# Kernel tuning notes

Hardware: AMD Instinct MI355X
Metric: run time of the kernel (lower is better)

## Reference

```python
import jax, jax.numpy as jnp
import numpy as np

N, C, K, B, G = 32768, 128, 16, 4, 8
SCALE, BASE = 2.0, 10000.0

def _bn(x, gamma, beta, eps=1e-5):
    # torch BatchNorm1d (training): stats over all axes except channel (last)
    axes = tuple(range(x.ndim - 1))
    mean = x.mean(axes)
    var = x.var(axes)
    return (x - mean) / jnp.sqrt(var + eps) * gamma + beta

def _cayley_rope(x, coord, S_param):
    c = x.shape[-1]
    S = jnp.triu(S_param, 1)
    S = S - S.T
    I = jnp.eye(c, dtype=x.dtype)
    P = jnp.linalg.solve(I + S, I - S)  # (I+S)^-1 (I-S)
    xr = x @ P.T
    dpa = c // 3 // 2 * 2          # dim per axis (even)
    dr = dpa * 3                   # rotated dims
    inv_freq = 1.0 / (BASE ** (jnp.arange(0, dpa, 2, dtype=jnp.float32) / dpa))
    cs = coord * SCALE
    def rot(f, c1):
        ang = c1[:, None] * inv_freq[None, :]
        s, co = jnp.sin(ang), jnp.cos(ang)
        fr, fi = jnp.split(f, 2, axis=-1)
        return jnp.concatenate([fr * co - fi * s, fr * s + fi * co], -1)
    parts = [rot(xr[:, i * dpa:(i + 1) * dpa], cs[:, i]) for i in range(3)]
    out = jnp.concatenate(parts + [xr[:, dr:]], -1)
    return out @ P

def setup_inputs() -> dict:
    key = jax.random.key(0)
    ks = jax.random.split(key, 24)
    w = lambda k, i, o, s=0.02: jax.random.normal(k, (i, o), jnp.float32) * s
    inp = {
        'feat': jax.random.normal(ks[0], (N, C), jnp.float32),
        'coord': jax.random.uniform(ks[1], (N, 3), jnp.float32) * 10.0,
        'reference_index': jax.random.randint(ks[2], (N, K), 0, N),
        'offset': jnp.arange(1, B + 1, dtype=jnp.int32) * (N // B),
        'Wq': w(ks[3], C, C), 'bq': jnp.zeros((C,)),
        'gq': jnp.ones((C,)), 'bnq': jnp.zeros((C,)),
        'Wk': w(ks[4], C, C), 'bk': jnp.zeros((C,)),
        'gk': jnp.ones((C,)), 'bnk': jnp.zeros((C,)),
        'Wv': w(ks[5], C, C), 'bv': jnp.zeros((C,)),
        'S_param': jax.random.normal(ks[6], (C, C), jnp.float32) * 0.01,
        'Ww1': w(ks[7], C, G), 'bw1': jnp.zeros((G,)),
        'gw': jnp.ones((G,)), 'bnw': jnp.zeros((G,)),
        'Ww2': w(ks[8], G, G), 'bw2': jnp.zeros((G,)),
        'Wg1': w(ks[9], 2 * C, C), 'bg1': jnp.zeros((C,)),
        'gg': jnp.ones((C,)), 'bng': jnp.zeros((C,)),
        'Wg2': w(ks[10], C, G, 0.001), 'bg2': jnp.full((G,), 3.0),
    }
    return inp

def reference(feat, coord, reference_index, offset, Wq, bq, gq, bnq, Wk, bk, gk, bnk,
              Wv, bv, S_param, Ww1, bw1, gw, bnw, Ww2, bw2, Wg1, bg1, gg, bng, Wg2, bg2):
    q_raw = jax.nn.relu(_bn(feat @ Wq + bq, gq, bnq))
    k_raw = jax.nn.relu(_bn(feat @ Wk + bk, gk, bnk))
    value = feat @ Wv + bv
    q = _cayley_rope(q_raw, coord, S_param)
    k = _cayley_rope(k_raw, coord, S_param)
    kg = k[reference_index]            # [N,K,C] gather
    vg = value[reference_index]        # [N,K,C]
    rel = kg - q[:, None, :]
    geom = jax.nn.relu(_bn(rel @ Ww1 + bw1, gw, bnw)) @ Ww2 + bw2  # [N,K,G]
    seg = jnp.searchsorted(offset, jnp.arange(N), side='right')
    gmax = jax.ops.segment_max(q_raw, seg, num_segments=B)
    gate_in = jnp.concatenate([q_raw, gmax[seg]], -1)              # [N,2C]
    gate = jax.nn.sigmoid(jax.nn.relu(_bn(gate_in @ Wg1 + bg1, gg, bng)) @ Wg2 + bg2)  # [N,G]
    refined = geom * (1.0 + gate[:, None, :])
    attn = jax.nn.softmax(refined, axis=1)
    mask = jnp.sign(reference_index + 1).astype(attn.dtype)
    attn = attn * mask[:, :, None]
    vg4 = vg.reshape(N, K, G, C // G)
    out = jnp.einsum('nkgi,nkg->ngi', vg4, attn).reshape(N, C)
    return out
```

## Files before the change

### kernel.cpp

```cpp
#include <hip/hip_runtime.h>
#include <math.h>

#define N_PTS 32768
#define C_DIM 128
#define K_NB  16
#define G_DIM 8

#define OF_PW     0
#define OF_STATQ  1024
#define OF_STATK  1280
#define OF_STATG1 1536
#define OF_STATH  1792
#define OF_UMAXP  1808
#define OF_UMAXN  2320
#define OF_GSG    2832
#define OF_WQT    4096
#define OF_WKT    12288
#define OF_WVT    20480
#define OF_WG1T   28672
#define OF_PTMIT  36864
#define OF_QW     65536
#define OF_KW     327680
#define OF_GATE   589824
#define OF_G1     1048576
#define OF_V      5242880

typedef short bf16x8 __attribute__((ext_vector_type(8)));
typedef float f32x4  __attribute__((ext_vector_type(4)));

#define LSTR 136

__device__ __forceinline__ unsigned f2bf(float f) {
  unsigned u = __float_as_uint(f);
  return (u + 0x7fffu + ((u >> 16) & 1u)) >> 16;
}
__device__ __forceinline__ float bf2f(short s) {
  return __uint_as_float(((unsigned)(unsigned short)s) << 16);
}
__device__ __forceinline__ unsigned fenc(float f) {
  unsigned b = __float_as_uint(f);
  return (b & 0x80000000u) ? ~b : (b | 0x80000000u);
}
__device__ __forceinline__ float fdec(unsigned u) {
  unsigned b = (u & 0x80000000u) ? (u & 0x7fffffffu) : ~u;
  return __uint_as_float(b);
}
__device__ __forceinline__ bf16x8 pack_bf8(float4 a, float4 b) {
  bf16x8 r;
  r[0] = (short)f2bf(a.x); r[1] = (short)f2bf(a.y);
  r[2] = (short)f2bf(a.z); r[3] = (short)f2bf(a.w);
  r[4] = (short)f2bf(b.x); r[5] = (short)f2bf(b.y);
  r[6] = (short)f2bf(b.z); r[7] = (short)f2bf(b.w);
  return r;
}

__device__ __forceinline__ void g2l16(const void* g, void* l) {
  __builtin_amdgcn_global_load_lds(
      (const __attribute__((address_space(1))) void*)g,
      (__attribute__((address_space(3))) void*)l, 16, 0, 0);
}

__device__ __forceinline__ void stage_async(short* dst, const short* __restrict__ src, int tid) {
  int lane = tid & 63, wv = tid >> 6;
  #pragma unroll
  for (int it = 0; it < 8; ++it) {
    int chunk = it*256 + wv*64;
    int D = (chunk + lane)*16;
    int gs = D ^ (((D >> 8) & 7) << 4);
    g2l16((const char*)src + gs, (char*)dst + chunk*16);
  }
}

__device__ __forceinline__ f32x4 mfma1(const short* Bb, const bf16x8* a4, int row, int quad) {
  f32x4 ac = {0.f, 0.f, 0.f, 0.f};
  int sx = (row & 7) << 4;
  #pragma unroll
  for (int ks = 0; ks < 4; ++ks) {
    const char* p = (const char*)Bb + (((row*256) + ks*64 + quad*16) ^ sx);
    ac = __builtin_amdgcn_mfma_f32_16x16x32_bf16(a4[ks], *(const bf16x8*)p, ac, 0, 0, 0);
  }
  return ac;
}

__global__ __launch_bounds__(256) void cayley(const float* __restrict__ Sp,
    const float* __restrict__ Ww1,
    const float* __restrict__ Wq, const float* __restrict__ Wk,
    const float* __restrict__ Wv, const float* __restrict__ Wg1,
    short* __restrict__ WqT, short* __restrict__ WkT,
    short* __restrict__ WvT, short* __restrict__ Wg1T,
    short* __restrict__ PTmIT, float* __restrict__ PW,
    float* __restrict__ statz)
{
  __shared__ __align__(16) short Ssh[128*LSTR];
  __shared__ float x0[128], x1[128];
  int bx = blockIdx.x, tid = threadIdx.x;
  if (bx >= 64) {
    if (bx < 80) {
      int idx = bx - 64, widx = idx >> 2, qr = idx & 3;
      const float* src = (widx == 0) ? Wq : (widx == 1) ? Wk : (widx == 2) ? Wv : Wg1;
      short* dst = (widx == 0) ? WqT : (widx == 1) ? WkT : (widx == 2) ? WvT : Wg1T;
      const float4* s4 = (const float4*)src;
      short* T = Ssh;
      #pragma unroll
      for (int it = 0; it < 4; ++it) {
        int q = it*256 + tid; int kloc = q >> 5, n4 = q & 31;
        float4 v = s4[(qr*32 + kloc)*32 + n4];
        T[(n4*4+0)*40 + kloc] = (short)f2bf(v.x);
        T[(n4*4+1)*40 + kloc] = (short)f2bf(v.y);
        T[(n4*4+2)*40 + kloc] = (short)f2bf(v.z);
        T[(n4*4+3)*40 + kloc] = (short)f2bf(v.w);
      }
      __syncthreads();
      #pragma unroll
      for (int it = 0; it < 2; ++it) {
        int i2 = it*256 + tid;
        int n = i2 >> 2, part = i2 & 3;
        uint4 val = *(const uint4*)&T[n*40 + part*8];
        *(uint4*)&dst[n*128 + qr*32 + part*8] = val;
      }
    } else {
      #pragma unroll
      for (int it = 0; it < 8; ++it) {
        int idx = it*256 + tid;
        if (idx < 1808) statz[idx] = 0.f;
      }
    }
    return;
  }
  int c0 = bx*2, c1 = c0 + 1;
  {
    const float4* s4 = (const float4*)Sp;
    #pragma unroll
    for (int it = 0; it < 16; ++it) {
      int idx = it*256 + tid;
      int i = idx >> 5, j0 = (idx & 31) * 4;
      float4 v = s4[idx];
      #pragma unroll
      for (int u = 0; u < 4; ++u) {
        int j = j0 + u;
        float val = (&v.x)[u];
        if (j > i) {
          unsigned b = f2bf(val);
          Ssh[i*LSTR + j] = (short)b;
          Ssh[j*LSTR + i] = (short)(b ^ 0x8000u);
        } else if (j == i) {
          Ssh[i*LSTR + j] = 0;
        }
      }
    }
  }
  if (tid < 128) {
    x0[tid] = (tid == c0) ? 1.f : 0.f;
    x1[tid] = (tid == c1) ? 1.f : 0.f;
  }
  __syncthreads();
  int i = tid >> 1, h = tid & 1;
  const short* srow = &Ssh[i*LSTR + h*64];
  for (int t = 0; t < 16; ++t) {
    float a0 = 0.f, a1 = 0.f;
    #pragma unroll
    for (int jq = 0; jq < 16; ++jq) {
      short4 sv = *(const short4*)&srow[jq*4];
      #pragma unroll
      for (int u = 0; u < 4; ++u) {
        float s = bf2f((&sv.x)[u]);
        int j = h*64 + jq*4 + u;
        a0 = fmaf(s, x0[j], a0);
        a1 = fmaf(s, x1[j], a1);
      }
    }
    a0 += __shfl_xor(a0, 1);
    a1 += __shfl_xor(a1, 1);
    __syncthreads();
    if (h == 0) {
      x0[i] = a0 + ((i == c0) ? 1.f : 0.f);
      x1[i] = a1 + ((i == c1) ? 1.f : 0.f);
    }
    __syncthreads();
  }
  if (tid < 128) {
    PTmIT[c0*128 + tid] = (short)f2bf(2.f*x0[tid] - ((tid == c0) ? 2.f : 0.f));
  } else {
    int t = tid - 128;
    PTmIT[c1*128 + t] = (short)f2bf(2.f*x1[t] - ((t == c1) ? 2.f : 0.f));
  }
  if (tid < 16) {
    int cc = tid >> 3, g = tid & 7;
    const float* xv = cc ? x1 : x0;
    int c = cc ? c1 : c0;
    float acc = 0.f;
    #pragma unroll 8
    for (int j = 0; j < 128; ++j) acc = fmaf(xv[j], Ww1[j*8 + g], acc);
    PW[c*8 + g] = 2.f*acc - Ww1[c*8 + g];
  }
}

__global__ __launch_bounds__(256, 2) void qkv_mfma(const float* __restrict__ feat,
    const short* __restrict__ WqT, const short* __restrict__ WkT, const short* __restrict__ WvT,
    const float* __restrict__ bq, const float* __restrict__ bk, const float* __restrict__ bv,
    float* __restrict__ Vv,
    float* __restrict__ statq, float* __restrict__ statk,
    unsigned* __restrict__ umaxp, unsigned* __restrict__ umaxn)
{
  __shared__ __align__(16) short Bb0[128*128];
  __shared__ __align__(16) short Bb1[128*128];
  __shared__ float ssum[2][128], ssq[2][128];
  __shared__ unsigned ump[128], umn[128];
  int tid = threadIdx.x, row0 = blockIdx.x * 64, seg = row0 >> 13;
  int lane = tid & 63, w = tid >> 6, l15 = lane & 15, quad = lane >> 4;
  stage_async(Bb0, WqT, tid);
  if (tid < 128) {
    ssum[0][tid] = 0.f; ssum[1][tid] = 0.f;
    ssq[0][tid] = 0.f;  ssq[1][tid] = 0.f;
    ump[tid] = 0u; umn[tid] = 0u;
  }
  bf16x8 af[4];
  {
    long rbase = (long)(row0 + w*16 + l15) * 128;
    #pragma unroll
    for (int ks = 0; ks < 4; ++ks) {
      int c0 = ks*32 + quad*8;
      float4 v0 = *(const float4*)&feat[rbase + c0];
      float4 v1 = *(const float4*)&feat[rbase + c0 + 4];
      af[ks] = pack_bf8(v0, v1);
    }
  }
  __syncthreads();
  stage_async(Bb1, WkT, tid);
  {
    #pragma unroll
    for (int nt = 0; nt < 8; ++nt) {
      f32x4 ac = mfma1(Bb0, af, nt*16 + l15, quad);
      int col = nt*16 + l15;
      float bb = bq[col];
      float s = 0.f, s2 = 0.f, mx = -1e30f, mn = 1e30f;
      #pragma unroll
      for (int r = 0; r < 4; ++r) {
        float raw = ac[r];
        float v = raw + bb;
        s += v; s2 = fmaf(v, v, s2);
        mx = fmaxf(mx, raw); mn = fminf(mn, raw);
      }
      s += __shfl_xor(s, 16); s += __shfl_xor(s, 32);
      s2 += __shfl_xor(s2, 16); s2 += __shfl_xor(s2, 32);
      mx = fmaxf(mx, __shfl_xor(mx, 16)); mx = fmaxf(mx, __shfl_xor(mx, 32));
      mn = fminf(mn, __shfl_xor(mn, 16)); mn = fminf(mn, __shfl_xor(mn, 32));
      if (lane < 16) {
        atomicAdd(&ssum[0][col], s); atomicAdd(&ssq[0][col], s2);
        atomicMax(&ump[col], fenc(mx)); atomicMax(&umn[col], fenc(-mn));
      }
    }
  }
  __syncthreads();
  stage_async(Bb0, WvT, tid);
  {
    #pragma unroll
    for (int nt = 0; nt < 8; ++nt) {
      f32x4 ac = mfma1(Bb1, af, nt*16 + l15, quad);
      int col = nt*16 + l15;
      float bb = bk[col];
      float s = 0.f, s2 = 0.f;
      #pragma unroll
      for (int r = 0; r < 4; ++r) {
        float v = ac[r] + bb;
        s += v; s2 = fmaf(v, v, s2);
      }
      s += __shfl_xor(s, 16); s += __shfl_xor(s, 32);
      s2 += __shfl_xor(s2, 16); s2 += __shfl_xor(s2, 32);
      if (lane < 16) { atomicAdd(&ssum[1][col], s); atomicAdd(&ssq[1][col], s2); }
    }
  }
  __syncthreads();
  {
    #pragma unroll
    for (int nt = 0; nt < 8; ++nt) {
      f32x4 ac = mfma1(Bb0, af, nt*16 + l15, quad);
      int col = nt*16 + l15;
      float bb = bv[col];
      #pragma unroll
      for (int r = 0; r < 4; ++r)
        Vv[(long)(row0 + w*16 + quad*4 + r)*128 + col] = ac[r] + bb;
    }
  }
  __syncthreads();
  if (tid < 128) {
    atomicAdd(&statq[tid], ssum[0][tid]); atomicAdd(&statq[128 + tid], ssq[0][tid]);
    atomicAdd(&statk[tid], ssum[1][tid]); atomicAdd(&statk[128 + tid], ssq[1][tid]);
    atomicMax(&umaxp[seg*128 + tid], ump[tid]);
    atomicMax(&umaxn[seg*128 + tid], umn[tid]);
  }
}

__global__ __launch_bounds__(128) void gprep(
    const float* __restrict__ statq,
    const float* __restrict__ gq, const float* __restrict__ bnq,
    const float* __restrict__ bq,
    const unsigned* __restrict__ umaxp, const unsigned* __restrict__ umaxn,
    const float* __restrict__ Wg1, const float* __restrict__ bg1,
    float* __restrict__ gsgO)
{
  __shared__ float gml[128];
  int s = blockIdx.x, tid = threadIdx.x;
  const float invn = 1.f / 32768.f;
  {
    float m = statq[tid]*invn, vv = fmaf(-m, m, statq[128 + tid]*invn);
    float a = rsqrtf(vv + 1e-5f) * gq[tid];
    float b = fmaf(-m, a, bnq[tid]);
    float cb2 = fmaf(a, bq[tid], b);
    float mx = fdec(umaxp[s*128 + tid]);
    float mn = -fdec(umaxn[s*128 + tid]);
    gml[tid] = fmaxf(0.f, fmaxf(fmaf(a, mx, cb2), fmaf(a, mn, cb2)));
  }
  __syncthreads();
  float acc = bg1[tid];
  #pragma unroll 8
  for (int j = 0; j < 128; ++j)
    acc = fmaf(gml[j], Wg1[(128 + j)*128 + tid], acc);
  gsgO[s*128 + tid] = acc;
}

__global__ __launch_bounds__(256, 2) void rqkw(
    const float* __restrict__ feat,
    const short* __restrict__ WqT, const short* __restrict__ WkT,
    const short* __restrict__ PTmIT, const short* __restrict__ Wg1T,
    const float* __restrict__ coord,
    const float* __restrict__ bq, const float* __restrict__ bk,
    const float* __restrict__ statq, const float* __restrict__ statk,
    const float* __restrict__ gq, const float* __restrict__ bnq,
    const float* __restrict__ gk, const float* __restrict__ bnk,
    const float* __restrict__ gsgG,
    const float* __restrict__ PW, const float* __restrict__ bw1,
    float* __restrict__ qw, float* __restrict__ kw,
    float* __restrict__ g1, float* __restrict__ statg1)
{
  __shared__ __align__(16) char arena[81920];
  short* Bb0  = (short*)arena;
  short* Bb1  = (short*)(arena + 32768);
  char*  bnqS = arena + 65536;
  char*  bnkS = arena + 73728;
  float* ssum = (float*)(arena + 65536);
  float* ssq  = (float*)(arena + 66048);
  float* xsq  = (float*)arena;
  float* xsk  = (float*)(arena + 16896);
  float* pws  = (float*)(arena + 33792);
  int tid = threadIdx.x, row0 = blockIdx.x * 32, seg = row0 >> 13;
  int lane = tid & 63, w = tid >> 6, l15 = lane & 15, quad = lane >> 4;
  bool isq = (w < 2);
  int rw = (w & 1) * 16;
  stage_async(Bb0, WqT, tid);
  stage_async(Bb1, WkT, tid);
  bf16x8 af[4];
  {
    long rbase = (long)(row0 + rw + l15) * 128;
    #pragma unroll
    for (int ks = 0; ks < 4; ++ks) {
      int c0 = ks*32 + quad*8;
      float4 v0 = *(const float4*)&feat[rbase + c0];
      float4 v1 = *(const float4*)&feat[rbase + c0 + 4];
      af[ks] = pack_bf8(v0, v1);
    }
  }
  float caR[8], cbR[8];
  {
    const float* stat = isq ? statq : statk;
    const float* gg   = isq ? gq : gk;
    const float* bn_  = isq ? bnq : bnk;
    const float* bb_  = isq ? bq : bk;
    const float invn = 1.f / 32768.f;
    #pragma unroll
    for (int nt = 0; nt < 8; ++nt) {
      int col = nt*16 + l15;
      float m = stat[col]*invn, vv = fmaf(-m, m, stat[128 + col]*invn);
      float a = rsqrtf(vv + 1e-5f) * gg[col];
      float b = fmaf(-m, a, bn_[col]);
      caR[nt] = a; cbR[nt] = fmaf(a, bb_[col], b);
    }
  }
  __syncthreads();
  float bnl[32];
  if (isq) {
    #pragma unroll
    for (int nt = 0; nt < 8; ++nt) {
      f32x4 ac = mfma1(Bb0, af, nt*16 + l15, quad);
      int col = nt*16 + l15;
      float A = caR[nt], B = cbR[nt];
      #pragma unroll
      for (int r = 0; r < 4; ++r) {
        float v = fmaxf(0.f, fmaf(A, ac[r], B));
        bnl[nt*4 + r] = v;
        int row = rw + quad*4 + r;
        int ba = (row*256 + col*2) ^ ((row & 7) << 4);
        *(short*)(bnqS + ba) = (short)f2bf(v);
      }
    }
  }
  __syncthreads();
  stage_async(Bb0, PTmIT, tid);
  if (!isq) {
    #pragma unroll
    for (int nt = 0; nt < 8; ++nt) {
      f32x4 ac = mfma1(Bb1, af, nt*16 + l15, quad);
      int col = nt*16 + l15;
      float A = caR[nt], B = cbR[nt];
      #pragma unroll
      for (int r = 0; r < 4; ++r) {
        float v = fmaxf(0.f, fmaf(A, ac[r], B));
        bnl[nt*4 + r] = v;
        int row = rw + quad*4 + r;
        int ba = (row*256 + col*2) ^ ((row & 7) << 4);
        *(short*)(bnkS + ba) = (short)f2bf(v);
      }
    }
  }
  __syncthreads();
  stage_async(Bb1, Wg1T, tid);
  bf16x8 af2[4];
  {
    const char* bs = isq ? bnqS : bnkS;
    int rowA = rw + l15, sx2 = (rowA & 7) << 4;
    #pragma unroll
    for (int ks = 0; ks < 4; ++ks)
      af2[ks] = *(const bf16x8*)(bs + ((rowA*256 + ks*64 + quad*16) ^ sx2));
  }
  float gsR[8];
  if (isq) {
    #pragma unroll
    for (int nt = 0; nt < 8; ++nt)
      gsR[nt] = gsgG[seg*128 + nt*16 + l15];
  }
  f32x4 accv[8];
  #pragma unroll
  for (int nt = 0; nt < 8; ++nt)
    accv[nt] = mfma1(Bb0, af2, nt*16 + l15, quad);
  __syncthreads();
  if (tid >= 128) {
    int c = tid - 128;
    ssum[c] = 0.f; ssq[c] = 0.f;
  }
  __syncthreads();
  if (isq) {
    #pragma unroll
    for (int nt = 0; nt < 8; ++nt) {
      f32x4 ac = mfma1(Bb1, af2, nt*16 + l15, quad);
      int col = nt*16 + l15;
      float gsv = gsR[nt];
      float s = 0.f, s2 = 0.f;
      #pragma unroll
      for (int r = 0; r < 4; ++r) {
        float v = ac[r] + gsv;
        g1[(long)(row0 + rw + quad*4 + r)*128 + col] = v;
        s += v; s2 = fmaf(v, v, s2);
      }
      s += __shfl_xor(s, 16); s += __shfl_xor(s, 32);
      s2 += __shfl_xor(s2, 16); s2 += __shfl_xor(s2, 32);
      if (lane < 16) { atomicAdd(&ssum[col], s); atomicAdd(&ssq[col], s2); }
    }
  }
  __syncthreads();
  {
    float* xs = isq ? xsq : xsk;
    #pragma unroll
    for (int nt = 0; nt < 8; ++nt) {
      int col = nt*16 + l15;
      #pragma unroll
      for (int r = 0; r < 4; ++r)
        xs[(rw + quad*4 + r)*132 + col] = accv[nt][r] + bnl[nt*4 + r];
    }
  }
  #pragma unroll
  for (int it = 0; it < 4; ++it) { int idx = tid + it*256; pws[idx] = PW[idx]; }
  if (tid < 128) {
    atomicAdd(&statg1[tid], ssum[tid]);
    atomicAdd(&statg1[128 + tid], ssq[tid]);
  }
  __syncthreads();
  #pragma unroll
  for (int it = 0; it < 8; ++it) {
    int idx = it*256 + tid;
    int r = idx >> 6, s = idx & 63;
    if (s < 63) {
      int a3 = s / 21, j = s - a3*21;
      int cr = a3*42 + j;
      float invf = exp2f((float)(2*j) * (-13.287712379549449f / 42.f));
      float ang = coord[(row0 + r)*3 + a3] * (2.0f * invf);
      float sn, co; sincosf(ang, &sn, &co);
      float fr = xsq[r*132 + cr], fi = xsq[r*132 + cr + 21];
      xsq[r*132 + cr]      = fr*co - fi*sn;
      xsq[r*132 + cr + 21] = fr*sn + fi*co;
      fr = xsk[r*132 + cr]; fi = xsk[r*132 + cr + 21];
      xsk[r*132 + cr]      = fr*co - fi*sn;
      xsk[r*132 + cr + 21] = fr*sn + fi*co;
    }
  }
  __syncthreads();
  #pragma unroll
  for (int it = 0; it < 2; ++it) {
    int idx = it*256 + tid;
    int mat = idx >> 8, r2 = (idx >> 3) & 31, g = idx & 7;
    const float* x2 = mat ? xsk : xsq;
    float a0 = 0.f, a1 = 0.f, a2 = 0.f, a3 = 0.f;
    #pragma unroll 8
    for (int i = 0; i < 128; i += 4) {
      float4 xv = *(const float4*)&x2[r2*132 + i];
      a0 = fmaf(xv.x, pws[(i+0)*8 + g], a0);
      a1 = fmaf(xv.y, pws[(i+1)*8 + g], a1);
      a2 = fmaf(xv.z, pws[(i+2)*8 + g], a2);
      a3 = fmaf(xv.w, pws[(i+3)*8 + g], a3);
    }
    float acc = (a0 + a1) + (a2 + a3) + (mat ? bw1[g] : 0.f);
    float* dst = mat ? kw : qw;
    dst[(long)(row0 + r2)*8 + g] = acc;
  }
}

__global__ __launch_bounds__(256) void mid(
    const float* __restrict__ g1, const float* __restrict__ statg1,
    const float* __restrict__ ggm, const float* __restrict__ bng,
    const float* __restrict__ Wg2, const float* __restrict__ bg2,
    float* __restrict__ gate,
    const float* __restrict__ kw, const float* __restrict__ qw,
    const int* __restrict__ ref, float* __restrict__ stath)
{
  __shared__ float gs[32][132];
  __shared__ float w2s[128][8];
  __shared__ float cA[128], cB[128];
  __shared__ float red[256];
  int tid = threadIdx.x;
  if (blockIdx.x < 1024) {
    int row0 = blockIdx.x * 32;
    #pragma unroll
    for (int it = 0; it < 4; ++it) { int idx = tid + it*256; w2s[idx >> 3][idx & 7] = Wg2[idx]; }
    if (tid < 128) {
      const float invn = 1.f / 32768.f;
      float m = statg1[tid]*invn, v = fmaf(-m, m, statg1[128 + tid]*invn);
      float a = rsqrtf(v + 1e-5f) * ggm[tid];
      cA[tid] = a; cB[tid] = fmaf(-m, a, bng[tid]);
    }
    #pragma unroll
    for (int it = 0; it < 4; ++it) {
      int idx = tid + it*256; int r = idx >> 5, cq = idx & 31;
      *(float4*)&gs[r][cq*4] = *(const float4*)&g1[(long)(row0 + r)*128 + cq*4];
    }
    __syncthreads();
    int r = tid >> 3, g = tid & 7;
    float acc = bg2[g];
    #pragma unroll 8
    for (int c2 = 0; c2 < 128; ++c2) {
      float act = fmaxf(0.f, fmaf(gs[r][c2], cA[c2], cB[c2]));
      acc = fmaf(act, w2s[c2][g], acc);
    }
    gate[(long)(row0 + r)*8 + g] = 1.f / (1.f + expf(-acc));
  } else {
    long base = (long)(blockIdx.x - 1024) * 4096;
    float s = 0.f, sq = 0.f;
    for (int it = 0; it < 16; ++it) {
      long idx = base + it*256 + tid;
      int n = (int)(idx >> 7); int kk = (int)((idx >> 3) & 15); int g = (int)(idx & 7);
      int r = ref[n*16 + kk];
      float h = kw[(long)r*8 + g] - qw[(long)n*8 + g];
      s += h; sq = fmaf(h, h, sq);
    }
    red[tid] = s; __syncthreads();
    for (int d = 128; d >= 8; d >>= 1) { if (tid < d) red[tid] += red[tid + d]; __syncthreads(); }
    if (tid < 8) atomicAdd(&stath[tid], red[tid]);
    __syncthreads();
    red[tid] = sq; __syncthreads();
    for (int d = 128; d >= 8; d >>= 1) { if (tid < d) red[tid] += red[tid + d]; __syncthreads(); }
    if (tid < 8) atomicAdd(&stath[8 + tid], red[tid]);
  }
}

__global__ __launch_bounds__(256) void attn_out(const float* __restrict__ qw, const float* __restrict__ kw,
                                                const float* __restrict__ stath,
                                                const float* __restrict__ gw, const float* __restrict__ bnw,
                                                const float* __restrict__ Ww2, const float* __restrict__ bw2,
                                                const float* __restrict__ gate, const int* __restrict__ ref,
                                                const float* __restrict__ v, float* __restrict__ out)
{
  __shared__ float sm1[2][16][9];
  __shared__ float sm2[2][16][9];
  __shared__ int   smr[2][16];
  int tid = threadIdx.x; int rh = tid >> 7, t = tid & 127;
  int n = blockIdx.x * 2 + rh;
  int kk = t >> 3, g = t & 7;
  if (t < 16) smr[rh][t] = ref[n*16 + t];
  __syncthreads();
  const float invnk = 1.f / 524288.f;
  float m0 = stath[g]*invnk, v0 = fmaf(-m0, m0, stath[8 + g]*invnk);
  float aw = rsqrtf(v0 + 1e-5f) * gw[g];
  float bw = fmaf(-m0, aw, bnw[g]);
  int rr = smr[rh][kk];
  float h = kw[(long)rr*8 + g] - qw[(long)n*8 + g];
  sm1[rh][kk][g] = fmaxf(0.f, fmaf(h, aw, bw));
  __syncthreads();
  float acc = bw2[g];
  #pragma unroll
  for (int g2 = 0; g2 < 8; ++g2) acc = fmaf(sm1[rh][kk][g2], Ww2[g2*8 + g], acc);
  float refined = acc * (1.f + gate[(long)n*8 + g]);
  sm2[rh][kk][g] = refined;
  __syncthreads();
  float mx = -1e30f;
  #pragma unroll
  for (int k2 = 0; k2 < 16; ++k2) mx = fmaxf(mx, sm2[rh][k2][g]);
  float e = expf(refined - mx);
  sm1[rh][kk][g] = e;
  __syncthreads();
  float ssum = 0.f;
  #pragma unroll
  for (int k2 = 0; k2 < 16; ++k2) ssum += sm1[rh][k2][g];
  float mask = ((rr + 1) > 0) ? 1.f : (((rr + 1) == 0) ? 0.f : -1.f);
  float attn = e / ssum * mask;
  sm2[rh][kk][g] = attn;
  __syncthreads();
  float o = 0.f;
  #pragma unroll
  for (int k2 = 0; k2 < 16; ++k2) {
    o = fmaf(v[(long)smr[rh][k2]*128 + t], sm2[rh][k2][t >> 4], o);
  }
  out[(long)n*128 + t] = o;
}

extern "C" void kernel_launch(void* const* d_in, const int* in_sizes, int n_in,
                              void* d_out, int out_size, void* d_ws, size_t ws_size,
                              hipStream_t stream)
{
  const float* feat  = (const float*)d_in[0];
  const float* coord = (const float*)d_in[1];
  const int*   ref   = (const int*)d_in[2];
  const float* Wq  = (const float*)d_in[4];
  const float* bq  = (const float*)d_in[5];
  const float* gq  = (const float*)d_in[6];
  const float* bnq = (const float*)d_in[7];
  const float* Wk  = (const float*)d_in[8];
  const float* bk  = (const float*)d_in[9];
  const float* gk  = (const float*)d_in[10];
  const float* bnk = (const float*)d_in[11];
  const float* Wv  = (const float*)d_in[12];
  const float* bv  = (const float*)d_in[13];
  const float* Sp  = (const float*)d_in[14];
  const float* Ww1 = (const float*)d_in[15];
  const float* bw1 = (const float*)d_in[16];
  const float* gw  = (const float*)d_in[17];
  const float* bnw = (const float*)d_in[18];
  const float* Ww2 = (const float*)d_in[19];
  const float* bw2 = (const float*)d_in[20];
  const float* Wg1 = (const float*)d_in[21];
  const float* bg1 = (const float*)d_in[22];
  const float* ggm = (const float*)d_in[23];
  const float* bng = (const float*)d_in[24];
  const float* Wg2 = (const float*)d_in[25];
  const float* bg2 = (const float*)d_in[26];
  float* out = (float*)d_out;

  float* W = (float*)d_ws;
  float* PW = W + OF_PW;
  short* WqT   = (short*)(W + OF_WQT);
  short* WkT   = (short*)(W + OF_WKT);
  short* WvT   = (short*)(W + OF_WVT);
  short* Wg1T  = (short*)(W + OF_WG1T);
  short* PTmIT = (short*)(W + OF_PTMIT);
  float* G1 = W + OF_G1;
  float* Vv = W + OF_V;

  cayley<<<81, 256, 0, stream>>>(Sp, Ww1, Wq, Wk, Wv, Wg1,
                                 WqT, WkT, WvT, Wg1T, PTmIT, PW, W + OF_STATQ);
  qkv_mfma<<<512, 256, 0, stream>>>(feat, WqT, WkT, WvT, bq, bk, bv, Vv,
                                    W + OF_STATQ, W + OF_STATK,
                                    (unsigned*)(W + OF_UMAXP), (unsigned*)(W + OF_UMAXN));
  gprep<<<4, 128, 0, stream>>>(W + OF_STATQ, gq, bnq, bq,
                               (const unsigned*)(W + OF_UMAXP),
                               (const unsigned*)(W + OF_UMAXN),
                               Wg1, bg1, W + OF_GSG);
  rqkw<<<1024, 256, 0, stream>>>(feat, WqT, WkT, PTmIT, Wg1T, coord,
                                 bq, bk,
                                 W + OF_STATQ, W + OF_STATK,
                                 gq, bnq, gk, bnk,
                                 W + OF_GSG, PW, bw1,
                                 W + OF_QW, W + OF_KW, G1, W + OF_STATG1);
  mid<<<2048, 256, 0, stream>>>(G1, W + OF_STATG1, ggm, bng, Wg2, bg2, W + OF_GATE,
                                W + OF_KW, W + OF_QW, ref, W + OF_STATH);
  attn_out<<<16384, 256, 0, stream>>>(W + OF_QW, W + OF_KW, W + OF_STATH, gw, bnw, Ww2, bw2,
                                      W + OF_GATE, ref, Vv, out);
}
```

Measured before the change: 303.9 us.

## Process 64 rows per rqkw block with every wave computing both Q and K

The rqkw kernel now handles 64 rows per block instead of 32, so each wave computes both the Q and K projections and Cayley transforms for its 16 rows rather than splitting waves between Q and K. This halves the block count and spreads the staged weight tiles (Wq, Wk, P, Wg1) over twice as many rows, cutting redundant LDS staging per row. The shared-memory column-stat atomics are replaced by per-wave partial sums combined in a plain reduction. In exchange, register pressure roughly doubles (two sets of BN coefficients, activations and accumulators), which may cause spills under launch_bounds(256,2), and 512 blocks give less parallelism.

```diff
diff --git a/kernel.cpp b/kernel.cpp
--- a/kernel.cpp
+++ b/kernel.cpp
@@ -336,22 +336,19 @@
   __shared__ __align__(16) char arena[81920];
   short* Bb0  = (short*)arena;
   short* Bb1  = (short*)(arena + 32768);
-  char*  bnqS = arena + 65536;
-  char*  bnkS = arena + 73728;
-  float* ssum = (float*)(arena + 65536);
-  float* ssq  = (float*)(arena + 66048);
+  char*  bnS  = arena + 65536;
   float* xsq  = (float*)arena;
-  float* xsk  = (float*)(arena + 16896);
-  float* pws  = (float*)(arena + 33792);
-  int tid = threadIdx.x, row0 = blockIdx.x * 32, seg = row0 >> 13;
+  float* xsk  = (float*)(arena + 33792);
+  float* pws  = (float*)(arena + 67584);
+  float* ssum4 = (float*)(arena + 71680);
+  float* ssq4  = (float*)(arena + 73728);
+  int tid = threadIdx.x, row0 = blockIdx.x * 64, seg = row0 >> 13;
   int lane = tid & 63, w = tid >> 6, l15 = lane & 15, quad = lane >> 4;
-  bool isq = (w < 2);
-  int rw = (w & 1) * 16;
   stage_async(Bb0, WqT, tid);
   stage_async(Bb1, WkT, tid);
   bf16x8 af[4];
   {
-    long rbase = (long)(row0 + rw + l15) * 128;
+    long rbase = (long)(row0 + w*16 + l15) * 128;
     #pragma unroll
     for (int ks = 0; ks < 4; ++ks) {
       int c0 = ks*32 + quad*8;
@@ -360,122 +357,142 @@
       af[ks] = pack_bf8(v0, v1);
     }
   }
-  float caR[8], cbR[8];
-  {
-    const float* stat = isq ? statq : statk;
-    const float* gg   = isq ? gq : gk;
-    const float* bn_  = isq ? bnq : bnk;
-    const float* bb_  = isq ? bq : bk;
+  float caRq[8], cbRq[8], caRk[8], cbRk[8];
+  {
     const float invn = 1.f / 32768.f;
     #pragma unroll
     for (int nt = 0; nt < 8; ++nt) {
       int col = nt*16 + l15;
-      float m = stat[col]*invn, vv = fmaf(-m, m, stat[128 + col]*invn);
-      float a = rsqrtf(vv + 1e-5f) * gg[col];
-      float b = fmaf(-m, a, bn_[col]);
-      caR[nt] = a; cbR[nt] = fmaf(a, bb_[col], b);
-    }
-  }
-  __syncthreads();
-  float bnl[32];
-  if (isq) {
+      float m = statq[col]*invn, vv = fmaf(-m, m, statq[128 + col]*invn);
+      float a = rsqrtf(vv + 1e-5f) * gq[col];
+      float b = fmaf(-m, a, bnq[col]);
+      caRq[nt] = a; cbRq[nt] = fmaf(a, bq[col], b);
+      m = statk[col]*invn; vv = fmaf(-m, m, statk[128 + col]*invn);
+      a = rsqrtf(vv + 1e-5f) * gk[col];
+      b = fmaf(-m, a, bnk[col]);
+      caRk[nt] = a; cbRk[nt] = fmaf(a, bk[col], b);
+    }
+  }
+  float gsR[8];
+  #pragma unroll
+  for (int nt = 0; nt < 8; ++nt)
+    gsR[nt] = gsgG[seg*128 + nt*16 + l15];
+  __syncthreads();
+  float bnl_q[32], bnl_k[32];
+  {
     #pragma unroll
     for (int nt = 0; nt < 8; ++nt) {
       f32x4 ac = mfma1(Bb0, af, nt*16 + l15, quad);
       int col = nt*16 + l15;
-      float A = caR[nt], B = cbR[nt];
+      float A = caRq[nt], B = cbRq[nt];
       #pragma unroll
       for (int r = 0; r < 4; ++r) {
         float v = fmaxf(0.f, fmaf(A, ac[r], B));
-        bnl[nt*4 + r] = v;
-        int row = rw + quad*4 + r;
+        bnl_q[nt*4 + r] = v;
+        int row = w*16 + quad*4 + r;
         int ba = (row*256 + col*2) ^ ((row & 7) << 4);
-        *(short*)(bnqS + ba) = (short)f2bf(v);
+        *(short*)(bnS + ba) = (short)f2bf(v);
       }
     }
   }
   __syncthreads();
   stage_async(Bb0, PTmIT, tid);
-  if (!isq) {
+  {
     #pragma unroll
     for (int nt = 0; nt < 8; ++nt) {
       f32x4 ac = mfma1(Bb1, af, nt*16 + l15, quad);
+      float A = caRk[nt], B = cbRk[nt];
+      #pragma unroll
+      for (int r = 0; r < 4; ++r)
+        bnl_k[nt*4 + r] = fmaxf(0.f, fmaf(A, ac[r], B));
+    }
+  }
+  __syncthreads();
+  stage_async(Bb1, Wg1T, tid);
+  bf16x8 af2q[4];
+  {
+    int rowA = w*16 + l15, sx2 = (rowA & 7) << 4;
+    #pragma unroll
+    for (int ks = 0; ks < 4; ++ks)
+      af2q[ks] = *(const bf16x8*)(bnS + ((rowA*256 + ks*64 + quad*16) ^ sx2));
+  }
+  f32x4 accv_q[8];
+  #pragma unroll
+  for (int nt = 0; nt < 8; ++nt)
+    accv_q[nt] = mfma1(Bb0, af2q, nt*16 + l15, quad);
+  __syncthreads();
+  {
+    #pragma unroll
+    for (int nt = 0; nt < 8; ++nt) {
       int col = nt*16 + l15;
-      float A = caR[nt], B = cbR[nt];
       #pragma unroll
       for (int r = 0; r < 4; ++r) {
-        float v = fmaxf(0.f, fmaf(A, ac[r], B));
-        bnl[nt*4 + r] = v;
-        int row = rw + quad*4 + r;
+        int row = w*16 + quad*4 + r;
         int ba = (row*256 + col*2) ^ ((row & 7) << 4);
-        *(short*)(bnkS + ba) = (short)f2bf(v);
-      }
-    }
-  }
-  __syncthreads();
-  stage_async(Bb1, Wg1T, tid);
-  bf16x8 af2[4];
-  {
-    const char* bs = isq ? bnqS : bnkS;
-    int rowA = rw + l15, sx2 = (rowA & 7) << 4;
+        *(short*)(bnS + ba) = (short)f2bf(bnl_k[nt*4 + r]);
+      }
+    }
+  }
+  __syncthreads();
+  bf16x8 af2k[4];
+  {
+    int rowA = w*16 + l15, sx2 = (rowA & 7) << 4;
     #pragma unroll
     for (int ks = 0; ks < 4; ++ks)
-      af2[ks] = *(const bf16x8*)(bs + ((rowA*256 + ks*64 + quad*16) ^ sx2));
-  }
-  float gsR[8];
-  if (isq) {
-    #pragma unroll
-    for (int nt = 0; nt < 8; ++nt)
-      gsR[nt] = gsgG[seg*128 + nt*16 + l15];
-  }
-  f32x4 accv[8];
-  #pragma unroll
-  for (int nt = 0; nt < 8; ++nt)
-    accv[nt] = mfma1(Bb0, af2, nt*16 + l15, quad);
-  __syncthreads();
-  if (tid >= 128) {
-    int c = tid - 128;
-    ssum[c] = 0.f; ssq[c] = 0.f;
-  }
-  __syncthreads();
-  if (isq) {
-    #pragma unroll
-    for (int nt = 0; nt < 8; ++nt) {
-      f32x4 ac = mfma1(Bb1, af2, nt*16 + l15, quad);
+      af2k[ks] = *(const bf16x8*)(bnS + ((rowA*256 + ks*64 + quad*16) ^ sx2));
+  }
+  f32x4 accv_k[8];
+  float sred[8], s2red[8];
+  {
+    #pragma unroll
+    for (int nt = 0; nt < 8; ++nt) {
+      accv_k[nt] = mfma1(Bb0, af2k, nt*16 + l15, quad);
+      f32x4 ac = mfma1(Bb1, af2q, nt*16 + l15, quad);
       int col = nt*16 + l15;
       float gsv = gsR[nt];
       float s = 0.f, s2 = 0.f;
       #pragma unroll
       for (int r = 0; r < 4; ++r) {
         float v = ac[r] + gsv;
-        g1[(long)(row0 + rw + quad*4 + r)*128 + col] = v;
+        g1[(long)(row0 + w*16 + quad*4 + r)*128 + col] = v;
         s += v; s2 = fmaf(v, v, s2);
       }
       s += __shfl_xor(s, 16); s += __shfl_xor(s, 32);
       s2 += __shfl_xor(s2, 16); s2 += __shfl_xor(s2, 32);
-      if (lane < 16) { atomicAdd(&ssum[col], s); atomicAdd(&ssq[col], s2); }
-    }
-  }
-  __syncthreads();
-  {
-    float* xs = isq ? xsq : xsk;
+      sred[nt] = s; s2red[nt] = s2;
+    }
+  }
+  __syncthreads();
+  {
     #pragma unroll
     for (int nt = 0; nt < 8; ++nt) {
       int col = nt*16 + l15;
       #pragma unroll
-      for (int r = 0; r < 4; ++r)
-        xs[(rw + quad*4 + r)*132 + col] = accv[nt][r] + bnl[nt*4 + r];
+      for (int r = 0; r < 4; ++r) {
+        int row = w*16 + quad*4 + r;
+        xsq[row*132 + col] = accv_q[nt][r] + bnl_q[nt*4 + r];
+        xsk[row*132 + col] = accv_k[nt][r] + bnl_k[nt*4 + r];
+      }
     }
   }
   #pragma unroll
   for (int it = 0; it < 4; ++it) { int idx = tid + it*256; pws[idx] = PW[idx]; }
+  if (lane < 16) {
+    #pragma unroll
+    for (int nt = 0; nt < 8; ++nt) {
+      ssum4[w*128 + nt*16 + l15] = sred[nt];
+      ssq4[w*128 + nt*16 + l15] = s2red[nt];
+    }
+  }
+  __syncthreads();
   if (tid < 128) {
-    atomicAdd(&statg1[tid], ssum[tid]);
-    atomicAdd(&statg1[128 + tid], ssq[tid]);
-  }
-  __syncthreads();
-  #pragma unroll
-  for (int it = 0; it < 8; ++it) {
+    float s = (ssum4[tid] + ssum4[128 + tid]) + (ssum4[256 + tid] + ssum4[384 + tid]);
+    float s2 = (ssq4[tid] + ssq4[128 + tid]) + (ssq4[256 + tid] + ssq4[384 + tid]);
+    atomicAdd(&statg1[tid], s);
+    atomicAdd(&statg1[128 + tid], s2);
+  }
+  #pragma unroll
+  for (int it = 0; it < 16; ++it) {
     int idx = it*256 + tid;
     int r = idx >> 6, s = idx & 63;
     if (s < 63) {
@@ -494,9 +511,9 @@
   }
   __syncthreads();
   #pragma unroll
-  for (int it = 0; it < 2; ++it) {
+  for (int it = 0; it < 4; ++it) {
     int idx = it*256 + tid;
-    int mat = idx >> 8, r2 = (idx >> 3) & 31, g = idx & 7;
+    int mat = idx >> 9, r2 = (idx >> 3) & 63, g = idx & 7;
     const float* x2 = mat ? xsk : xsq;
     float a0 = 0.f, a1 = 0.f, a2 = 0.f, a3 = 0.f;
     #pragma unroll 8
@@ -671,12 +688,12 @@
                                (const unsigned*)(W + OF_UMAXP),
                                (const unsigned*)(W + OF_UMAXN),
                                Wg1, bg1, W + OF_GSG);
-  rqkw<<<1024, 256, 0, stream>>>(feat, WqT, WkT, PTmIT, Wg1T, coord,
-                                 bq, bk,
-                                 W + OF_STATQ, W + OF_STATK,
-                                 gq, bnq, gk, bnk,
-                                 W + OF_GSG, PW, bw1,
-                                 W + OF_QW, W + OF_KW, G1, W + OF_STATG1);
+  rqkw<<<512, 256, 0, stream>>>(feat, WqT, WkT, PTmIT, Wg1T, coord,
+                                bq, bk,
+                                W + OF_STATQ, W + OF_STATK,
+                                gq, bnq, gk, bnk,
+                                W + OF_GSG, PW, bw1,
+                                W + OF_QW, W + OF_KW, G1, W + OF_STATG1);
   mid<<<2048, 256, 0, stream>>>(G1, W + OF_STATG1, ggm, bng, Wg2, bg2, W + OF_GATE,
                                 W + OF_KW, W + OF_QW, ref, W + OF_STATH);
   attn_out<<<16384, 256, 0, stream>>>(W + OF_QW, W + OF_KW, W + OF_STATH, gw, bnw, Ww2, bw2,
```

New measurement: 290.1 us, median of 2. 1.05x faster.
